# Performance work log

Hardware: AMD Instinct MI355X
Metric: run time of the kernel (lower is better)

Reference implementation:

```python
import jax, jax.numpy as jnp
import numpy as np

C, T, H, W, K = 12, 10, 4, 7, 3  # hardcoded in the original forward
PAD = 1
EPS = 1e-5


def setup_inputs() -> dict:
    key = jax.random.key(0)
    ks = jax.random.split(key, 14)
    nt = 32768
    x = jax.random.normal(ks[0], (nt, C, T, H * W), jnp.float32)
    # G: Linear(T -> 2T) -> BN1d(2T) -> ReLU -> Linear(2T -> K) -> Softmax
    w_g1 = jax.random.normal(ks[1], (2 * T, T), jnp.float32) * 0.3
    g1_gamma = 1.0 + 0.1 * jax.random.normal(ks[2], (2 * T,), jnp.float32)
    g1_beta = 0.1 * jax.random.normal(ks[3], (2 * T,), jnp.float32)
    g1_mean = 0.1 * jax.random.normal(ks[4], (2 * T,), jnp.float32)
    g1_var = jax.random.uniform(ks[5], (2 * T,), jnp.float32, 0.5, 1.5)
    w_g2 = jax.random.normal(ks[6], (K, 2 * T), jnp.float32) * 0.3
    # L: Conv1d(C -> C//4, K) -> BN1d(C//4) -> ReLU -> Conv1d(C//4 -> C, 1) -> Sigmoid
    w_l1 = jax.random.normal(ks[7], (C // 4, C, K), jnp.float32) * 0.3
    l1_gamma = 1.0 + 0.1 * jax.random.normal(ks[8], (C // 4,), jnp.float32)
    l1_beta = 0.1 * jax.random.normal(ks[9], (C // 4,), jnp.float32)
    l1_mean = 0.1 * jax.random.normal(ks[10], (C // 4,), jnp.float32)
    l1_var = jax.random.uniform(ks[11], (C // 4,), jnp.float32, 0.5, 1.5)
    w_l2 = jax.random.normal(ks[12], (C, C // 4, 1), jnp.float32) * 0.3
    return dict(x=x, w_g1=w_g1, g1_gamma=g1_gamma, g1_beta=g1_beta,
                g1_mean=g1_mean, g1_var=g1_var, w_g2=w_g2, w_l1=w_l1,
                l1_gamma=l1_gamma, l1_beta=l1_beta, l1_mean=l1_mean,
                l1_var=l1_var, w_l2=w_l2)


def reference(x, w_g1, g1_gamma, g1_beta, g1_mean, g1_var, w_g2,
              w_l1, l1_gamma, l1_beta, l1_mean, l1_var, w_l2):
    n = x.shape[0]
    new_x = x.reshape(n, C, T, H, W)
    # adaptive_avg_pool2d((1,1)) == mean over spatial dims -> [n, C, T]
    pooled = new_x.mean(axis=(3, 4))
    # --- G branch: per-(sample,channel) temporal kernel, [n, C, K] ---
    rows = pooled.reshape(n * C, T)
    z = rows @ w_g1.T
    z = (z - g1_mean) * jax.lax.rsqrt(g1_var + EPS) * g1_gamma + g1_beta
    z = jax.nn.relu(z)
    kern = jax.nn.softmax(z @ w_g2.T, axis=-1).reshape(n, C, K)
    # --- L branch: local channel-temporal gating, [n, C, T] ---
    a = jax.lax.conv_general_dilated(pooled, w_l1, (1,), [(K // 2, K // 2)],
                                     dimension_numbers=('NCH', 'OIH', 'NCH'))
    a = (a - l1_mean[None, :, None]) * jax.lax.rsqrt(l1_var + EPS)[None, :, None] \
        * l1_gamma[None, :, None] + l1_beta[None, :, None]
    a = jax.nn.relu(a)
    a = jax.lax.conv_general_dilated(a, w_l2, (1,), [(0, 0)],
                                     dimension_numbers=('NCH', 'OIH', 'NCH'))
    act = jax.nn.sigmoid(a)  # [n, C, T]
    # --- modulate and apply per-(sample,channel) depthwise temporal conv ---
    xm = new_x * act[:, :, :, None, None]  # [n, C, T, H, W]
    xp = jnp.pad(xm, ((0, 0), (0, 0), (PAD, PAD), (0, 0), (0, 0)))
    out = kern[:, :, 0, None, None, None] * xp[:, :, 0:T]
    for j in range(1, K):  # K=3, tiny structural loop
        out = out + kern[:, :, j, None, None, None] * xp[:, :, j:j + T]
    # permute [n,c,t,h,w] -> [n,t,c,h,w] and flatten time into batch
    out = jnp.transpose(out, (0, 2, 1, 3, 4)).reshape(n * T, C, H, W)
    return out
```

## Files before the change

### kernel.cpp

```cpp
#include <hip/hip_runtime.h>


#define CC 12
#define TT 10
#define HWS 28
#define SAMPLE 3360
#define SAMPLE4 840
#define EPSF 1e-5f

typedef float f4 __attribute__((ext_vector_type(4)));

#define WSYNC() do { asm volatile("s_waitcnt lgkmcnt(0)" ::: "memory"); \
                     __builtin_amdgcn_sched_barrier(0); } while (0)

__global__ __launch_bounds__(64) void tam_kernel(
    const float* __restrict__ x,
    const float* __restrict__ w_g1,
    const float* __restrict__ g1_gamma, const float* __restrict__ g1_beta,
    const float* __restrict__ g1_mean,  const float* __restrict__ g1_var,
    const float* __restrict__ w_g2,
    const float* __restrict__ w_l1,
    const float* __restrict__ l1_gamma, const float* __restrict__ l1_beta,
    const float* __restrict__ l1_mean,  const float* __restrict__ l1_var,
    const float* __restrict__ w_l2,
    float* __restrict__ out)
{
    __shared__ f4    sx4[SAMPLE4];
    __shared__ float spool[CC * TT];
    __shared__ float sz[CC * 2 * TT];
    __shared__ float sa1[3 * TT];
    __shared__ f4    skern[CC];
    __shared__ float sact[CC * TT];
    __shared__ f4    sw4[CC * TT];

    const int n    = blockIdx.x;
    const int lane = threadIdx.x;

    const f4* xg = reinterpret_cast<const f4*>(x + (size_t)n * SAMPLE);
    f4 r[13];
    #pragma unroll
    for (int k = 0; k < 13; ++k)
        r[k] = __builtin_nontemporal_load(xg + k * 64 + lane);
    f4 rt = (f4)0.f;
    if (lane < 8) rt = __builtin_nontemporal_load(xg + 832 + lane);
    #pragma unroll
    for (int k = 0; k < 13; ++k) sx4[k * 64 + lane] = r[k];
    if (lane < 8) sx4[832 + lane] = rt;
    WSYNC();

    #pragma unroll
    for (int rr = 0; rr < 2; ++rr) {
        const int row = lane + rr * 64;
        if (row < CC * TT) {
            const f4* rp = sx4 + row * 7;
            f4 a = rp[0];
            #pragma unroll
            for (int i = 1; i < 7; ++i) a += rp[i];
            spool[row] = (a.x + a.y + a.z + a.w) * (1.0f / 28.0f);
        }
    }
    WSYNC();

    #pragma unroll
    for (int q = 0; q < 5; ++q) {
        const int task = lane + q * 64;
        if (task < 240) {
            const int c = task / 20, j = task % 20;
            float s = 0.f;
            #pragma unroll
            for (int t = 0; t < TT; ++t) s += spool[c * TT + t] * w_g1[j * TT + t];
            s = (s - g1_mean[j]) * rsqrtf(g1_var[j] + EPSF) * g1_gamma[j] + g1_beta[j];
            sz[task] = fmaxf(s, 0.f);
        } else if (task < 270) {
            const int e = task - 240;
            const int m = e / TT, t = e % TT;
            float s = 0.f;
            #pragma unroll
            for (int c = 0; c < CC; ++c) {
                #pragma unroll
                for (int k = 0; k < 3; ++k) {
                    const int t2 = t + k - 1;
                    if (t2 >= 0 && t2 < TT)
                        s += spool[c * TT + t2] * w_l1[(m * CC + c) * 3 + k];
                }
            }
            s = (s - l1_mean[m]) * rsqrtf(l1_var[m] + EPSF) * l1_gamma[m] + l1_beta[m];
            sa1[e] = fmaxf(s, 0.f);
        }
    }
    WSYNC();

    if (lane < CC) {
        const int c = lane;
        float sc0 = 0.f, sc1 = 0.f, sc2 = 0.f;
        #pragma unroll
        for (int j = 0; j < 20; ++j) {
            const float zj = sz[c * 20 + j];
            sc0 += zj * w_g2[j];
            sc1 += zj * w_g2[20 + j];
            sc2 += zj * w_g2[40 + j];
        }
        const float mx = fmaxf(sc0, fmaxf(sc1, sc2));
        const float e0 = __expf(sc0 - mx), e1 = __expf(sc1 - mx), e2 = __expf(sc2 - mx);
        const float ri = 1.0f / (e0 + e1 + e2);
        f4 kk; kk.x = e0 * ri; kk.y = e1 * ri; kk.z = e2 * ri; kk.w = 0.f;
        skern[c] = kk;
    }
    #pragma unroll
    for (int q = 0; q < 2; ++q) {
        const int task = lane + q * 64;
        if (task < CC * TT) {
            const int c = task / TT, t = task % TT;
            float s = 0.f;
            #pragma unroll
            for (int m = 0; m < 3; ++m) s += sa1[m * TT + t] * w_l2[c * 3 + m];
            sact[task] = 1.0f / (1.0f + __expf(-s));
        }
    }
    WSYNC();

    #pragma unroll
    for (int q = 0; q < 2; ++q) {
        const int task = lane + q * 64;
        if (task < CC * TT) {
            const int c = task / TT, t = task % TT;
            const f4 kk = skern[c];
            f4 w;
            w.x = (t > 0) ? kk.x * sact[c * TT + t - 1] : 0.f;
            w.y = kk.y * sact[c * TT + t];
            w.z = (t < 9) ? kk.z * sact[c * TT + t + 1] : 0.f;
            w.w = 0.f;
            sw4[task] = w;
        }
    }
    WSYNC();

    f4* og = reinterpret_cast<f4*>(out + (size_t)n * SAMPLE);
    #pragma unroll
    for (int k = 0; k < 14; ++k) {
        const int vo = lane + k * 64;
        if (k < 13 || lane < 8) {
            const int t   = vo / 84;
            const int rem = vo % 84;
            const int c   = rem / 7;
            const int s4  = rem % 7;
            const f4 w = sw4[c * TT + t];
            const int base = c * 70 + s4;
            const int tm = (t > 0) ? t - 1 : 0;
            const int tp = (t < 9) ? t + 1 : 9;
            const f4 x0 = sx4[base + tm * 7];
            const f4 x1 = sx4[base + t * 7];
            const f4 x2 = sx4[base + tp * 7];
            const f4 acc = w.x * x0 + w.y * x1 + w.z * x2;
            og[vo] = acc;
        }
    }
}

extern "C" void kernel_launch(void* const* d_in, const int* in_sizes, int n_in,
                              void* d_out, int out_size, void* d_ws, size_t ws_size,
                              hipStream_t stream) {
    (void)n_in; (void)out_size; (void)d_ws; (void)ws_size;
    const float* x        = (const float*)d_in[0];
    const float* w_g1     = (const float*)d_in[1];
    const float* g1_gamma = (const float*)d_in[2];
    const float* g1_beta  = (const float*)d_in[3];
    const float* g1_mean  = (const float*)d_in[4];
    const float* g1_var   = (const float*)d_in[5];
    const float* w_g2     = (const float*)d_in[6];
    const float* w_l1     = (const float*)d_in[7];
    const float* l1_gamma = (const float*)d_in[8];
    const float* l1_beta  = (const float*)d_in[9];
    const float* l1_mean  = (const float*)d_in[10];
    const float* l1_var   = (const float*)d_in[11];
    const float* w_l2     = (const float*)d_in[12];
    float* out = (float*)d_out;

    const int n_total = in_sizes[0] / SAMPLE;
    tam_kernel<<<n_total, 64, 0, stream>>>(
        x, w_g1, g1_gamma, g1_beta, g1_mean, g1_var, w_g2,
        w_l1, l1_gamma, l1_beta, l1_mean, l1_var, w_l2, out);
}
```

Before: 238.4 us.

## Persistent 4-wave blocks, reduce LDS footprint, re-read x from cache for output

Switches from one 64-thread block per sample to 1024 persistent 256-thread blocks in which each wave loops over a contiguous run of samples. Weights and folded BN scale/shift are staged in LDS once per block. Instead of keeping the whole sample in LDS, each wave stores only per-float4 partial sums for pooling and re-reads x from global/L2 for the output convolution. This shrinks LDS per sample and amortizes setup, but reads x roughly three extra times through cache, removes the nontemporal loads and caps the grid at 4096 waves.

```diff
diff --git a/kernel.cpp b/kernel.cpp
--- a/kernel.cpp
+++ b/kernel.cpp
@@ -3,9 +3,7 @@
 
 #define CC 12
 #define TT 10
-#define HWS 28
 #define SAMPLE 3360
-#define SAMPLE4 840
 #define EPSF 1e-5f
 
 typedef float f4 __attribute__((ext_vector_type(4)));
@@ -13,7 +11,17 @@
 #define WSYNC() do { asm volatile("s_waitcnt lgkmcnt(0)" ::: "memory"); \
                      __builtin_amdgcn_sched_barrier(0); } while (0)
 
-__global__ __launch_bounds__(64) void tam_kernel(
+#define WS_F    1024
+#define OFF_SZ    0
+#define OFF_SA1 240
+#define OFF_SACT 272
+#define OFF_SW0 400
+#define OFF_SW1 520
+#define OFF_SW2 640
+#define OFF_POOL 840
+#define OFF_SK  960
+
+__global__ __launch_bounds__(256, 4) void tam_kernel(
     const float* __restrict__ x,
     const float* __restrict__ w_g1,
     const float* __restrict__ g1_gamma, const float* __restrict__ g1_beta,
@@ -23,137 +31,163 @@
     const float* __restrict__ l1_gamma, const float* __restrict__ l1_beta,
     const float* __restrict__ l1_mean,  const float* __restrict__ l1_var,
     const float* __restrict__ w_l2,
-    float* __restrict__ out)
+    float* __restrict__ out, int n_total, int iters)
 {
-    __shared__ f4    sx4[SAMPLE4];
-    __shared__ float spool[CC * TT];
-    __shared__ float sz[CC * 2 * TT];
-    __shared__ float sa1[3 * TT];
-    __shared__ f4    skern[CC];
-    __shared__ float sact[CC * TT];
-    __shared__ f4    sw4[CC * TT];
-
-    const int n    = blockIdx.x;
-    const int lane = threadIdx.x;
-
-    const f4* xg = reinterpret_cast<const f4*>(x + (size_t)n * SAMPLE);
-    f4 r[13];
-    #pragma unroll
-    for (int k = 0; k < 13; ++k)
-        r[k] = __builtin_nontemporal_load(xg + k * 64 + lane);
-    f4 rt = (f4)0.f;
-    if (lane < 8) rt = __builtin_nontemporal_load(xg + 832 + lane);
-    #pragma unroll
-    for (int k = 0; k < 13; ++k) sx4[k * 64 + lane] = r[k];
-    if (lane < 8) sx4[832 + lane] = rt;
-    WSYNC();
-
-    #pragma unroll
-    for (int rr = 0; rr < 2; ++rr) {
-        const int row = lane + rr * 64;
-        if (row < CC * TT) {
-            const f4* rp = sx4 + row * 7;
-            f4 a = rp[0];
-            #pragma unroll
-            for (int i = 1; i < 7; ++i) a += rp[i];
-            spool[row] = (a.x + a.y + a.z + a.w) * (1.0f / 28.0f);
-        }
+    __shared__ float sscr[4 * WS_F];
+    __shared__ float wg1[200], wg2[60], wl1[108], wl2[36];
+    __shared__ float gsS[20], gbS[20], lsS[3], lbS[3];
+
+    const int tid = threadIdx.x;
+
+    for (int i = tid; i < 200; i += 256) wg1[i] = w_g1[i];
+    for (int i = tid; i < 60;  i += 256) wg2[i] = w_g2[i];
+    for (int i = tid; i < 108; i += 256) wl1[i] = w_l1[i];
+    for (int i = tid; i < 36;  i += 256) wl2[i] = w_l2[i];
+    if (tid < 20) {
+        const float s = rsqrtf(g1_var[tid] + EPSF) * g1_gamma[tid];
+        gsS[tid] = s; gbS[tid] = g1_beta[tid] - g1_mean[tid] * s;
+    } else if (tid < 23) {
+        const int m = tid - 20;
+        const float s = rsqrtf(l1_var[m] + EPSF) * l1_gamma[m];
+        lsS[m] = s; lbS[m] = l1_beta[m] - l1_mean[m] * s;
     }
-    WSYNC();
-
-    #pragma unroll
-    for (int q = 0; q < 5; ++q) {
-        const int task = lane + q * 64;
-        if (task < 240) {
-            const int c = task / 20, j = task % 20;
+    __syncthreads();
+
+    const int wid  = tid >> 6;
+    const int lane = tid & 63;
+    float* ws = sscr + wid * WS_F;
+    const int gw = blockIdx.x * 4 + wid;
+
+    for (int it = 0; it < iters; ++it) {
+        const int n = gw * iters + it;
+        if (n >= n_total) break;
+        const f4* xg = reinterpret_cast<const f4*>(x + (size_t)n * SAMPLE);
+        f4*       og = reinterpret_cast<f4*>(out + (size_t)n * SAMPLE);
+
+        f4 r[13];
+        #pragma unroll
+        for (int k = 0; k < 13; ++k) r[k] = xg[k * 64 + lane];
+        f4 rt;
+        if (lane < 8) rt = xg[832 + lane];
+        #pragma unroll
+        for (int k = 0; k < 13; ++k)
+            ws[k * 64 + lane] = r[k].x + r[k].y + r[k].z + r[k].w;
+        if (lane < 8) ws[832 + lane] = rt.x + rt.y + rt.z + rt.w;
+        WSYNC();
+
+        {
+            const int r0 = lane;
             float s = 0.f;
             #pragma unroll
-            for (int t = 0; t < TT; ++t) s += spool[c * TT + t] * w_g1[j * TT + t];
-            s = (s - g1_mean[j]) * rsqrtf(g1_var[j] + EPSF) * g1_gamma[j] + g1_beta[j];
-            sz[task] = fmaxf(s, 0.f);
-        } else if (task < 270) {
-            const int e = task - 240;
-            const int m = e / TT, t = e % TT;
-            float s = 0.f;
+            for (int i = 0; i < 7; ++i) s += ws[r0 * 7 + i];
+            ws[OFF_POOL + r0] = s * (1.0f / 28.0f);
+            if (lane < 56) {
+                const int r1 = lane + 64;
+                float s1 = 0.f;
+                #pragma unroll
+                for (int i = 0; i < 7; ++i) s1 += ws[r1 * 7 + i];
+                ws[OFF_POOL + r1] = s1 * (1.0f / 28.0f);
+            }
+        }
+        WSYNC();
+
+        #pragma unroll
+        for (int q = 0; q < 5; ++q) {
+            const int task = lane + q * 64;
+            if (task < 240) {
+                const int c = task / 20, j = task % 20;
+                float s = 0.f;
+                #pragma unroll
+                for (int t = 0; t < TT; ++t)
+                    s += ws[OFF_POOL + c * TT + t] * wg1[j * TT + t];
+                ws[OFF_SZ + task] = fmaxf(gsS[j] * s + gbS[j], 0.f);
+            } else if (task < 270) {
+                const int e = task - 240;
+                const int m = e / TT, t = e % TT;
+                float s = 0.f;
+                #pragma unroll
+                for (int c = 0; c < CC; ++c) {
+                    #pragma unroll
+                    for (int k = 0; k < 3; ++k) {
+                        const int t2 = t + k - 1;
+                        if (t2 >= 0 && t2 < TT)
+                            s += ws[OFF_POOL + c * TT + t2] * wl1[(m * CC + c) * 3 + k];
+                    }
+                }
+                ws[OFF_SA1 + e] = fmaxf(lsS[m] * s + lbS[m], 0.f);
+            }
+        }
+        WSYNC();
+
+        if (lane < CC) {
+            const int c = lane;
+            float sc0 = 0.f, sc1 = 0.f, sc2 = 0.f;
             #pragma unroll
-            for (int c = 0; c < CC; ++c) {
-                #pragma unroll
-                for (int k = 0; k < 3; ++k) {
-                    const int t2 = t + k - 1;
-                    if (t2 >= 0 && t2 < TT)
-                        s += spool[c * TT + t2] * w_l1[(m * CC + c) * 3 + k];
-                }
-            }
-            s = (s - l1_mean[m]) * rsqrtf(l1_var[m] + EPSF) * l1_gamma[m] + l1_beta[m];
-            sa1[e] = fmaxf(s, 0.f);
-        }
-    }
-    WSYNC();
-
-    if (lane < CC) {
-        const int c = lane;
-        float sc0 = 0.f, sc1 = 0.f, sc2 = 0.f;
-        #pragma unroll
-        for (int j = 0; j < 20; ++j) {
-            const float zj = sz[c * 20 + j];
-            sc0 += zj * w_g2[j];
-            sc1 += zj * w_g2[20 + j];
-            sc2 += zj * w_g2[40 + j];
-        }
-        const float mx = fmaxf(sc0, fmaxf(sc1, sc2));
-        const float e0 = __expf(sc0 - mx), e1 = __expf(sc1 - mx), e2 = __expf(sc2 - mx);
-        const float ri = 1.0f / (e0 + e1 + e2);
-        f4 kk; kk.x = e0 * ri; kk.y = e1 * ri; kk.z = e2 * ri; kk.w = 0.f;
-        skern[c] = kk;
-    }
-    #pragma unroll
-    for (int q = 0; q < 2; ++q) {
-        const int task = lane + q * 64;
-        if (task < CC * TT) {
-            const int c = task / TT, t = task % TT;
-            float s = 0.f;
-            #pragma unroll
-            for (int m = 0; m < 3; ++m) s += sa1[m * TT + t] * w_l2[c * 3 + m];
-            sact[task] = 1.0f / (1.0f + __expf(-s));
-        }
-    }
-    WSYNC();
-
-    #pragma unroll
-    for (int q = 0; q < 2; ++q) {
-        const int task = lane + q * 64;
-        if (task < CC * TT) {
-            const int c = task / TT, t = task % TT;
-            const f4 kk = skern[c];
-            f4 w;
-            w.x = (t > 0) ? kk.x * sact[c * TT + t - 1] : 0.f;
-            w.y = kk.y * sact[c * TT + t];
-            w.z = (t < 9) ? kk.z * sact[c * TT + t + 1] : 0.f;
-            w.w = 0.f;
-            sw4[task] = w;
-        }
-    }
-    WSYNC();
-
-    f4* og = reinterpret_cast<f4*>(out + (size_t)n * SAMPLE);
-    #pragma unroll
-    for (int k = 0; k < 14; ++k) {
-        const int vo = lane + k * 64;
-        if (k < 13 || lane < 8) {
-            const int t   = vo / 84;
-            const int rem = vo % 84;
-            const int c   = rem / 7;
-            const int s4  = rem % 7;
-            const f4 w = sw4[c * TT + t];
-            const int base = c * 70 + s4;
-            const int tm = (t > 0) ? t - 1 : 0;
-            const int tp = (t < 9) ? t + 1 : 9;
-            const f4 x0 = sx4[base + tm * 7];
-            const f4 x1 = sx4[base + t * 7];
-            const f4 x2 = sx4[base + tp * 7];
-            const f4 acc = w.x * x0 + w.y * x1 + w.z * x2;
-            og[vo] = acc;
-        }
+            for (int j = 0; j < 20; ++j) {
+                const float zj = ws[OFF_SZ + c * 20 + j];
+                sc0 += zj * wg2[j];
+                sc1 += zj * wg2[20 + j];
+                sc2 += zj * wg2[40 + j];
+            }
+            const float mx = fmaxf(sc0, fmaxf(sc1, sc2));
+            const float e0 = __expf(sc0 - mx), e1 = __expf(sc1 - mx), e2 = __expf(sc2 - mx);
+            const float ri = 1.0f / (e0 + e1 + e2);
+            ws[OFF_SK + c]      = e0 * ri;
+            ws[OFF_SK + 12 + c] = e1 * ri;
+            ws[OFF_SK + 24 + c] = e2 * ri;
+        }
+        #pragma unroll
+        for (int q = 0; q < 2; ++q) {
+            const int task = lane + q * 64;
+            if (task < CC * TT) {
+                const int c = task / TT, t = task % TT;
+                float s = 0.f;
+                #pragma unroll
+                for (int m = 0; m < 3; ++m)
+                    s += ws[OFF_SA1 + m * TT + t] * wl2[c * 3 + m];
+                ws[OFF_SACT + task] = 1.0f / (1.0f + __expf(-s));
+            }
+        }
+        WSYNC();
+
+        #pragma unroll
+        for (int q = 0; q < 2; ++q) {
+            const int task = lane + q * 64;
+            if (task < CC * TT) {
+                const int c = task / TT, t = task % TT;
+                const float k0 = ws[OFF_SK + c];
+                const float k1 = ws[OFF_SK + 12 + c];
+                const float k2 = ws[OFF_SK + 24 + c];
+                ws[OFF_SW0 + task] = (t > 0) ? k0 * ws[OFF_SACT + c * TT + t - 1] : 0.f;
+                ws[OFF_SW1 + task] = k1 * ws[OFF_SACT + c * TT + t];
+                ws[OFF_SW2 + task] = (t < 9) ? k2 * ws[OFF_SACT + c * TT + t + 1] : 0.f;
+            }
+        }
+        WSYNC();
+
+        #pragma unroll
+        for (int k = 0; k < 14; ++k) {
+            const int vo = lane + k * 64;
+            if (k < 13 || lane < 8) {
+                const int t   = vo / 84;
+                const int rem = vo % 84;
+                const int c   = rem / 7;
+                const int s4  = rem % 7;
+                const int base = c * 70 + s4;
+                const int tm = (t > 0) ? t - 1 : 0;
+                const int tp = (t < 9) ? t + 1 : 9;
+                const f4 x0 = xg[base + tm * 7];
+                const f4 x1 = xg[base + t  * 7];
+                const f4 x2 = xg[base + tp * 7];
+                const int ct = c * TT + t;
+                const float w0 = ws[OFF_SW0 + ct];
+                const float w1 = ws[OFF_SW1 + ct];
+                const float w2 = ws[OFF_SW2 + ct];
+                const f4 acc = w0 * x0 + w1 * x1 + w2 * x2;
+                __builtin_nontemporal_store(acc, og + vo);
+            }
+        }
+        WSYNC();
     }
 }
 
@@ -167,8 +201,8 @@
     const float* g1_beta  = (const float*)d_in[3];
     const float* g1_mean  = (const float*)d_in[4];
     const float* g1_var   = (const float*)d_in[5];
+    const float* w_l1     = (const float*)d_in[7];
     const float* w_g2     = (const float*)d_in[6];
-    const float* w_l1     = (const float*)d_in[7];
     const float* l1_gamma = (const float*)d_in[8];
     const float* l1_beta  = (const float*)d_in[9];
     const float* l1_mean  = (const float*)d_in[10];
@@ -177,7 +211,10 @@
     float* out = (float*)d_out;
 
     const int n_total = in_sizes[0] / SAMPLE;
-    tam_kernel<<<n_total, 64, 0, stream>>>(
+    const int blocks  = 1024;
+    const int slots   = blocks * 4;
+    const int iters   = (n_total + slots - 1) / slots;
+    tam_kernel<<<blocks, 256, 0, stream>>>(
         x, w_g1, g1_gamma, g1_beta, g1_mean, g1_var, w_g2,
-        w_l1, l1_gamma, l1_beta, l1_mean, l1_var, w_l2, out);
+        w_l1, l1_gamma, l1_beta, l1_mean, l1_var, w_l2, out, n_total, iters);
 }
```

Result: slower. 279.8 us (+17.3%).

## Keep sample data in registers, process two samples per 256-thread block

Applied to the files above, without the earlier changes.

Restructures the kernel so each 128-thread half-block handles one sample. Each thread holds one (channel, spatial-vec4) column across all ten time steps in registers instead of staging the whole sample through LDS, and the pooling uses 8-lane shuffles. Weights and folded batch-norm scale/bias are staged once in shared memory, and the output is computed directly from registers. This removes large LDS traffic and frees occupancy, in exchange for idle lanes (c>=12, s4==7), strided non-coalesced loads and full __syncthreads barriers.

```diff
diff --git a/kernel.cpp b/kernel.cpp
--- a/kernel.cpp
+++ b/kernel.cpp
@@ -3,17 +3,12 @@
 
 #define CC 12
 #define TT 10
-#define HWS 28
 #define SAMPLE 3360
-#define SAMPLE4 840
 #define EPSF 1e-5f
 
 typedef float f4 __attribute__((ext_vector_type(4)));
 
-#define WSYNC() do { asm volatile("s_waitcnt lgkmcnt(0)" ::: "memory"); \
-                     __builtin_amdgcn_sched_barrier(0); } while (0)
-
-__global__ __launch_bounds__(64) void tam_kernel(
+__global__ __launch_bounds__(256, 6) void tam_kernel(
     const float* __restrict__ x,
     const float* __restrict__ w_g1,
     const float* __restrict__ g1_gamma, const float* __restrict__ g1_beta,
@@ -23,136 +18,122 @@
     const float* __restrict__ l1_gamma, const float* __restrict__ l1_beta,
     const float* __restrict__ l1_mean,  const float* __restrict__ l1_var,
     const float* __restrict__ w_l2,
-    float* __restrict__ out)
+    float* __restrict__ out, int n_total)
 {
-    __shared__ f4    sx4[SAMPLE4];
-    __shared__ float spool[CC * TT];
-    __shared__ float sz[CC * 2 * TT];
-    __shared__ float sa1[3 * TT];
-    __shared__ f4    skern[CC];
-    __shared__ float sact[CC * TT];
-    __shared__ f4    sw4[CC * TT];
+    __shared__ float wg1[200], wg2[60], wl1[108], wl2[36];
+    __shared__ float gs[20], gb[20], lsb[6];
+    __shared__ float pooled[2][120];
+    __shared__ float zz[2][240];
+    __shared__ float sa1[2][30];
+    __shared__ float sact[2][120];
+    __shared__ float skk[2][36];
 
-    const int n    = blockIdx.x;
-    const int lane = threadIdx.x;
+    const int tid  = threadIdx.x;
+    const int smp  = tid >> 7;
+    const int lane = tid & 127;
+    const int c    = lane >> 3;
+    const int s4   = lane & 7;
+    const int n    = blockIdx.x * 2 + smp;
+    const bool alive = (c < CC) && (s4 < 7) && (n < n_total);
 
     const f4* xg = reinterpret_cast<const f4*>(x + (size_t)n * SAMPLE);
-    f4 r[13];
+    f4 xv[TT];
     #pragma unroll
-    for (int k = 0; k < 13; ++k)
-        r[k] = __builtin_nontemporal_load(xg + k * 64 + lane);
-    f4 rt = (f4)0.f;
-    if (lane < 8) rt = __builtin_nontemporal_load(xg + 832 + lane);
-    #pragma unroll
-    for (int k = 0; k < 13; ++k) sx4[k * 64 + lane] = r[k];
-    if (lane < 8) sx4[832 + lane] = rt;
-    WSYNC();
+    for (int t = 0; t < TT; ++t) xv[t] = (f4)0.f;
+    if (alive) {
+        const int base = c * 70 + s4;
+        #pragma unroll
+        for (int t = 0; t < TT; ++t) xv[t] = xg[base + t * 7];
+    }
+
+    for (int i = tid; i < 200; i += 256) wg1[i] = w_g1[i];
+    if (tid < 60)  wg2[tid] = w_g2[tid];
+    if (tid < 108) wl1[tid] = w_l1[tid];
+    if (tid < 36)  wl2[tid] = w_l2[tid];
+    if (tid < 20) {
+        const float s = rsqrtf(g1_var[tid] + EPSF) * g1_gamma[tid];
+        gs[tid] = s; gb[tid] = g1_beta[tid] - g1_mean[tid] * s;
+    } else if (tid < 23) {
+        const int m = tid - 20;
+        const float s = rsqrtf(l1_var[m] + EPSF) * l1_gamma[m];
+        lsb[m] = s; lsb[3 + m] = l1_beta[m] - l1_mean[m] * s;
+    }
 
     #pragma unroll
-    for (int rr = 0; rr < 2; ++rr) {
-        const int row = lane + rr * 64;
-        if (row < CC * TT) {
-            const f4* rp = sx4 + row * 7;
-            f4 a = rp[0];
-            #pragma unroll
-            for (int i = 1; i < 7; ++i) a += rp[i];
-            spool[row] = (a.x + a.y + a.z + a.w) * (1.0f / 28.0f);
-        }
+    for (int t = 0; t < TT; ++t) {
+        float h = xv[t].x + xv[t].y + xv[t].z + xv[t].w;
+        h += __shfl_xor(h, 1, 8);
+        h += __shfl_xor(h, 2, 8);
+        h += __shfl_xor(h, 4, 8);
+        if (s4 == 0 && c < CC) pooled[smp][c * TT + t] = h * (1.0f / 28.0f);
     }
-    WSYNC();
+    __syncthreads();
 
     #pragma unroll
-    for (int q = 0; q < 5; ++q) {
-        const int task = lane + q * 64;
+    for (int q = 0; q < 3; ++q) {
+        const int task = lane + q * 128;
         if (task < 240) {
-            const int c = task / 20, j = task % 20;
+            const int cc = task / 20, j = task % 20;
             float s = 0.f;
             #pragma unroll
-            for (int t = 0; t < TT; ++t) s += spool[c * TT + t] * w_g1[j * TT + t];
-            s = (s - g1_mean[j]) * rsqrtf(g1_var[j] + EPSF) * g1_gamma[j] + g1_beta[j];
-            sz[task] = fmaxf(s, 0.f);
+            for (int t = 0; t < TT; ++t)
+                s += pooled[smp][cc * TT + t] * wg1[j * TT + t];
+            zz[smp][task] = fmaxf(gs[j] * s + gb[j], 0.f);
         } else if (task < 270) {
             const int e = task - 240;
             const int m = e / TT, t = e % TT;
             float s = 0.f;
             #pragma unroll
-            for (int c = 0; c < CC; ++c) {
+            for (int cc = 0; cc < CC; ++cc) {
                 #pragma unroll
                 for (int k = 0; k < 3; ++k) {
                     const int t2 = t + k - 1;
                     if (t2 >= 0 && t2 < TT)
-                        s += spool[c * TT + t2] * w_l1[(m * CC + c) * 3 + k];
+                        s += pooled[smp][cc * TT + t2] * wl1[(m * CC + cc) * 3 + k];
                 }
             }
-            s = (s - l1_mean[m]) * rsqrtf(l1_var[m] + EPSF) * l1_gamma[m] + l1_beta[m];
-            sa1[e] = fmaxf(s, 0.f);
+            sa1[smp][e] = fmaxf(lsb[m] * s + lsb[3 + m], 0.f);
         }
     }
-    WSYNC();
+    __syncthreads();
 
     if (lane < CC) {
-        const int c = lane;
         float sc0 = 0.f, sc1 = 0.f, sc2 = 0.f;
         #pragma unroll
         for (int j = 0; j < 20; ++j) {
-            const float zj = sz[c * 20 + j];
-            sc0 += zj * w_g2[j];
-            sc1 += zj * w_g2[20 + j];
-            sc2 += zj * w_g2[40 + j];
+            const float zj = zz[smp][lane * 20 + j];
+            sc0 += zj * wg2[j];
+            sc1 += zj * wg2[20 + j];
+            sc2 += zj * wg2[40 + j];
         }
         const float mx = fmaxf(sc0, fmaxf(sc1, sc2));
         const float e0 = __expf(sc0 - mx), e1 = __expf(sc1 - mx), e2 = __expf(sc2 - mx);
         const float ri = 1.0f / (e0 + e1 + e2);
-        f4 kk; kk.x = e0 * ri; kk.y = e1 * ri; kk.z = e2 * ri; kk.w = 0.f;
-        skern[c] = kk;
+        skk[smp][lane]      = e0 * ri;
+        skk[smp][12 + lane] = e1 * ri;
+        skk[smp][24 + lane] = e2 * ri;
     }
-    #pragma unroll
-    for (int q = 0; q < 2; ++q) {
-        const int task = lane + q * 64;
-        if (task < CC * TT) {
-            const int c = task / TT, t = task % TT;
-            float s = 0.f;
-            #pragma unroll
-            for (int m = 0; m < 3; ++m) s += sa1[m * TT + t] * w_l2[c * 3 + m];
-            sact[task] = 1.0f / (1.0f + __expf(-s));
-        }
+    if (lane < 120) {
+        const int cc = lane / TT, t = lane % TT;
+        float s = 0.f;
+        #pragma unroll
+        for (int m = 0; m < 3; ++m) s += sa1[smp][m * TT + t] * wl2[cc * 3 + m];
+        sact[smp][lane] = 1.0f / (1.0f + __expf(-s));
     }
-    WSYNC();
+    __syncthreads();
 
-    #pragma unroll
-    for (int q = 0; q < 2; ++q) {
-        const int task = lane + q * 64;
-        if (task < CC * TT) {
-            const int c = task / TT, t = task % TT;
-            const f4 kk = skern[c];
-            f4 w;
-            w.x = (t > 0) ? kk.x * sact[c * TT + t - 1] : 0.f;
-            w.y = kk.y * sact[c * TT + t];
-            w.z = (t < 9) ? kk.z * sact[c * TT + t + 1] : 0.f;
-            w.w = 0.f;
-            sw4[task] = w;
-        }
-    }
-    WSYNC();
-
-    f4* og = reinterpret_cast<f4*>(out + (size_t)n * SAMPLE);
-    #pragma unroll
-    for (int k = 0; k < 14; ++k) {
-        const int vo = lane + k * 64;
-        if (k < 13 || lane < 8) {
-            const int t   = vo / 84;
-            const int rem = vo % 84;
-            const int c   = rem / 7;
-            const int s4  = rem % 7;
-            const f4 w = sw4[c * TT + t];
-            const int base = c * 70 + s4;
-            const int tm = (t > 0) ? t - 1 : 0;
-            const int tp = (t < 9) ? t + 1 : 9;
-            const f4 x0 = sx4[base + tm * 7];
-            const f4 x1 = sx4[base + t * 7];
-            const f4 x2 = sx4[base + tp * 7];
-            const f4 acc = w.x * x0 + w.y * x1 + w.z * x2;
-            og[vo] = acc;
+    if (alive) {
+        f4* og = reinterpret_cast<f4*>(out + (size_t)n * SAMPLE);
+        const float k0 = skk[smp][c];
+        const float k1 = skk[smp][12 + c];
+        const float k2 = skk[smp][24 + c];
+        const float* ac = &sact[smp][c * TT];
+        #pragma unroll
+        for (int t = 0; t < TT; ++t) {
+            f4 r = (k1 * ac[t]) * xv[t];
+            if (t > 0)      r += (k0 * ac[t - 1]) * xv[t - 1];
+            if (t < TT - 1) r += (k2 * ac[t + 1]) * xv[t + 1];
+            og[t * 84 + c * 7 + s4] = r;
         }
     }
 }
@@ -177,7 +158,8 @@
     float* out = (float*)d_out;
 
     const int n_total = in_sizes[0] / SAMPLE;
-    tam_kernel<<<n_total, 64, 0, stream>>>(
+    const int blocks  = (n_total + 1) / 2;
+    tam_kernel<<<blocks, 256, 0, stream>>>(
         x, w_g1, g1_gamma, g1_beta, g1_mean, g1_var, w_g2,
-        w_l1, l1_gamma, l1_beta, l1_mean, l1_var, w_l2, out);
+        w_l1, l1_gamma, l1_beta, l1_mean, l1_var, w_l2, out, n_total);
 }
```

Result: no change. 239.9 us (+0.6%).
